# Kernel optimization log

Measured on AMD Instinct MI355X. Metric: run time of the kernel, lower is better.

Reference implementation:

```python
import jax, jax.numpy as jnp
import numpy as np

B, T, C, HS = 8, 2048, 1024, 64
SCALE = C ** (-0.5)  # NOTE: source scales by C, not head_size
NEG_INF = float('-inf')
NEG_BIG = -1e9


def setup_inputs() -> dict:
    key = jax.random.key(0)
    kV, kK, kQ, kWq, kWk, kWv, kL = jax.random.split(key, 7)
    V = jax.random.normal(kV, (B, T, C), dtype=jnp.float32)
    K = jax.random.normal(kK, (B, T, C), dtype=jnp.float32)
    Q = jax.random.normal(kQ, (B, T, C), dtype=jnp.float32)
    w_scale = 1.0 / np.sqrt(C)
    Wq = jax.random.normal(kWq, (C, HS), dtype=jnp.float32) * w_scale
    Wk = jax.random.normal(kWk, (C, HS), dtype=jnp.float32) * w_scale
    Wv = jax.random.normal(kWv, (C, HS), dtype=jnp.float32) * w_scale
    # padding only at the tail; valid lengths in [T//2, T] so no NaN softmax rows
    lengths = jax.random.randint(kL, (B,), T // 2, T + 1)
    pad_mask = (jnp.arange(T)[None, None, :] >= lengths[:, None, None])  # [B,1,T] bool
    return {"V": V, "K": K, "Q": Q, "Wq": Wq, "Wk": Wk, "Wv": Wv, "pad_mask": pad_mask}


def reference(V, K, Q, Wq, Wk, Wv, pad_mask):
    q = Q @ Wq  # [B,T,HS]
    k = K @ Wk
    v = V @ Wv
    A = jnp.einsum('btd,bsd->bts', q, k) * SCALE  # [B,T,T]
    t = A.shape[1]
    causal = jnp.triu(jnp.ones((t, A.shape[2]), dtype=bool), k=1)  # tril==0
    A = jnp.where(causal[None], NEG_INF, A)
    A = jnp.where(pad_mask, NEG_INF, A)  # mask padded key columns
    A = jnp.where(jnp.swapaxes(pad_mask, -2, -1)[:, :t, :], NEG_BIG, A)  # padded query rows
    A = jax.nn.softmax(A, axis=-1)
    return A @ v  # [B,T,HS]
```

## Files before the change

kernel.cpp:

```cpp
#include <hip/hip_runtime.h>
#include <hip/hip_bf16.h>

typedef short bf16x8 __attribute__((ext_vector_type(8)));
typedef float f32x4 __attribute__((ext_vector_type(4)));
typedef unsigned int u32;
typedef u32 u32x4 __attribute__((ext_vector_type(4)));

#define T_SEQ 2048
#define NB 8
#define NEGB (-1e30f)

__device__ inline unsigned short f2bf(float f) {
  unsigned u = __builtin_bit_cast(unsigned, f);
  u += 0x7FFFu + ((u >> 16) & 1u);
  return (unsigned short)(u >> 16);
}
__device__ inline float bf2f(unsigned short h) {
  unsigned u = ((unsigned)h) << 16;
  return __builtin_bit_cast(float, u);
}
__device__ inline u32 cvt2(float a, float b) {
  __hip_bfloat162 h = __float22bfloat162_rn(make_float2(a, b));
  u32 r;
  __builtin_memcpy(&r, &h, 4);
  return r;
}
__device__ inline bf16x8 pack8(float4 a, float4 b) {
  u32x4 p;
  p[0] = cvt2(a.x, a.y);
  p[1] = cvt2(a.z, a.w);
  p[2] = cvt2(b.x, b.y);
  p[3] = cvt2(b.z, b.w);
  return __builtin_bit_cast(bf16x8, p);
}
__device__ inline f32x4 mfma16(bf16x8 a, bf16x8 b, f32x4 c) {
  return __builtin_amdgcn_mfma_f32_16x16x32_bf16(a, b, c, 0, 0, 0);
}
__device__ __forceinline__ void gl_lds16(const void* g, void* l) {
  __builtin_amdgcn_global_load_lds(
      (const __attribute__((address_space(1))) void*)g,
      (__attribute__((address_space(3))) void*)l, 16, 0, 0);
}

__global__ void prep_k(const float* Wq, const float* Wk, const float* Wv,
                       unsigned short* wt, const unsigned char* m,
                       int* lengths, float* vmsum) {
  int tid = threadIdx.x;
  if (blockIdx.x < 768) {
    int e = blockIdx.x * 256 + tid;
    int mi = e >> 16;
    int rem = e & 65535;
    int kk = rem & 1023, n = rem >> 10;
    const float* W = (mi == 0) ? Wq : (mi == 1) ? Wk : Wv;
    wt[e] = f2bf(W[kk * 64 + n]);
    return;
  }
  int b = blockIdx.x - 768;
  if (tid < 64) vmsum[b * 64 + tid] = 0.f;
  int lo = 0, lb = 0;
  for (int i = tid; i < NB * T_SEQ; i += 256) {
    int v = (m[i] != 0);
    lo += v;
    if (i & 3) lb += v;
  }
  for (int off = 32; off >= 1; off >>= 1) {
    lo += __shfl_xor(lo, off);
    lb += __shfl_xor(lb, off);
  }
  __shared__ int s0[4], s1[4], ws2[4];
  if ((tid & 63) == 0) { s0[tid >> 6] = lo; s1[tid >> 6] = lb; }
  __syncthreads();
  int ones = s0[0] + s0[1] + s0[2] + s0[3];
  int bad = s1[0] + s1[1] + s1[2] + s1[3];
  int flag = (ones > 0 && bad == 0);
  int cnt = 0;
  if (flag) {
    const int* mi2 = (const int*)m;
    for (int t = tid; t < T_SEQ; t += 256) cnt += (mi2[b * T_SEQ + t] == 0);
  } else {
    for (int t = tid; t < T_SEQ; t += 256) cnt += (m[b * T_SEQ + t] == 0);
  }
  for (int off = 32; off >= 1; off >>= 1) cnt += __shfl_xor(cnt, off);
  __syncthreads();
  if ((tid & 63) == 0) ws2[tid >> 6] = cnt;
  __syncthreads();
  if (tid == 0) lengths[b] = ws2[0] + ws2[1] + ws2[2] + ws2[3];
}

__global__ __launch_bounds__(512, 4) void proj_k(
    const float* Q, const float* K, const float* V, const unsigned short* wt,
    unsigned short* qo, unsigned short* ko, unsigned short* vTb, float* vmsum) {
  __shared__ float xs[2][4096];
  __shared__ unsigned short wss[2][4096];
  int mi = blockIdx.y;
  const float* X = (mi == 0) ? Q : (mi == 1) ? K : V;
  const unsigned short* wtm = wt + mi * 65536;
  int tid = threadIdx.x;
  int w = tid >> 6, lane = tid & 63, l15 = lane & 15, g = lane >> 4;
  int wr = w >> 1, wc = w & 1;
  int r0b = blockIdx.x * 64;

  int segA = w * 2;
  int rowA0 = segA * 4 + (lane >> 4);
  int rowA1 = rowA0 + 4;
  int colA0 = ((lane & 15) ^ (rowA0 & 15)) * 4;
  int colA1 = ((lane & 15) ^ (rowA1 & 15)) * 4;
  const float* srcA0 = X + (size_t)(r0b + rowA0) * 1024 + colA0;
  const float* srcA1 = X + (size_t)(r0b + rowA1) * 1024 + colA1;
  int nW = w * 8 + (lane >> 3);
  int skW = ((lane & 7) ^ (nW & 7)) * 8;
  const unsigned short* srcW = wtm + (size_t)nW * 1024 + skW;

  f32x4 acc[2];
  acc[0] = 0; acc[1] = 0;

#define STAGE(buf, kc2)                                          \
  do {                                                           \
    gl_lds16(srcA0 + (kc2) * 64, &xs[buf][segA * 256]);          \
    gl_lds16(srcA1 + (kc2) * 64, &xs[buf][segA * 256 + 256]);    \
    gl_lds16(srcW + (kc2) * 64, &wss[buf][w * 512]);             \
  } while (0)

  STAGE(0, 0);

  int arow = wr * 16 + l15;
  for (int kc = 0; kc < 16; ++kc) {
    int cur = kc & 1;
    if (kc < 15) {
      STAGE(cur ^ 1, kc + 1);
      asm volatile("s_waitcnt vmcnt(3)" ::: "memory");
    } else {
      asm volatile("s_waitcnt vmcnt(0)" ::: "memory");
    }
    __builtin_amdgcn_s_barrier();
#pragma unroll
    for (int ks = 0; ks < 2; ++ks) {
      int lb0 = ks * 8 + g * 2;
      float4 fa = *(const float4*)&xs[cur][arow * 64 + ((lb0 ^ l15) * 4)];
      float4 fb = *(const float4*)&xs[cur][arow * 64 + (((lb0 + 1) ^ l15) * 4)];
      bf16x8 a = pack8(fa, fb);
#pragma unroll
      for (int nt = 0; nt < 2; ++nt) {
        int nrow = wc * 32 + nt * 16 + l15;
        bf16x8 bb = *(const bf16x8*)
            &wss[cur][nrow * 64 + (((ks * 4 + g) ^ (l15 & 7)) * 8)];
        acc[nt] = mfma16(a, bb, acc[nt]);
      }
    }
    if (kc < 15) {
      asm volatile("s_waitcnt lgkmcnt(0)" ::: "memory");
      __builtin_amdgcn_s_barrier();
    }
  }
#undef STAGE

#pragma unroll
  for (int nt = 0; nt < 2; ++nt)
#pragma unroll
    for (int vv = 0; vv < 4; ++vv) {
      int rr = r0b + wr * 16 + g * 4 + vv;
      int c = wc * 32 + nt * 16 + l15;
      float val = acc[nt][vv];
      if (mi == 0) {
        qo[(size_t)rr * 64 + c] = f2bf(val * 0.03125f);
      } else if (mi == 1) {
        ko[(size_t)rr * 64 + c] = f2bf(val);
      } else {
        int bb = rr >> 11, ts = rr & 2047;
        vTb[(((size_t)bb * 64 + (ts >> 5)) * 64 + c) * 32 + (ts & 31)] =
            f2bf(val);
      }
    }

  if (mi == 2) {
    float ps0 = acc[0][0] + acc[0][1] + acc[0][2] + acc[0][3];
    float ps1 = acc[1][0] + acc[1][1] + acc[1][2] + acc[1][3];
    __syncthreads();
    float* rb = (float*)xs;
    rb[(wc * 32 + l15) * 16 + (wr * 4 + g)] = ps0;
    rb[(wc * 32 + 16 + l15) * 16 + (wr * 4 + g)] = ps1;
    __syncthreads();
    if (tid < 64) {
      float s = 0.f;
#pragma unroll
      for (int i = 0; i < 16; ++i) s += rb[tid * 16 + i];
      atomicAdd(&vmsum[(blockIdx.x >> 5) * 64 + tid], s);
    }
  }
}

__global__ __launch_bounds__(512, 4) void attn_k(
    const unsigned short* q, const unsigned short* k, const unsigned short* vTb,
    const float* vmsum, const int* lengths, float* Out) {
  __shared__ unsigned short pL[8][16][40];
  __shared__ unsigned short oP[4][2][16][64];
  __shared__ float mP[4][2][16], lP[4][2][16];

  int id = blockIdx.x;
  int raw = id & 63, b = id >> 6;
  int xx = (raw + 8 * b) & 63;
  int tile = (xx < 32) ? xx : 95 - xx;
  int t0 = tile * 32;

  int tid = threadIdx.x;
  int w = tid >> 6, lane = tid & 63;
  int j = w >> 1, r = w & 1;
  int l15 = lane & 15, g = lane >> 4;
  int t_base = t0 + r * 16;

  const bf16x8* qrow =
      (const bf16x8*)(q + ((size_t)b * T_SEQ + t_base + l15) * 64);
  bf16x8 aq0 = qrow[g];
  bf16x8 aq1 = qrow[4 + g];

  f32x4 o[4];
  float m[4], l[4];
#pragma unroll
  for (int i = 0; i < 4; ++i) { o[i] = 0; m[i] = NEGB; l[i] = 0.f; }

  const bf16x8* kch = (const bf16x8*)k + (size_t)b * T_SEQ * 8;
  const unsigned short* vch = vTb + (size_t)b * 131072;

  int NT = tile + 1;
  int qn = NT >> 2, rem = NT & 3;
  int start = j * qn + (j < rem ? j : rem);
  int end = start + qn + (j < rem ? 1 : 0);
  int capw = ((t_base + 15) >> 5) + 1;
  if (end > capw) end = capw;

  bf16x8 kb00, kb01, kb10, kb11, bv0, bv1, bv2, bv3;
  if (start < end) {
    int s0 = start * 32;
    kb00 = kch[(size_t)(s0 + l15) * 8 + g];
    kb01 = kch[(size_t)(s0 + l15) * 8 + 4 + g];
    kb10 = kch[(size_t)(s0 + 16 + l15) * 8 + g];
    kb11 = kch[(size_t)(s0 + 16 + l15) * 8 + 4 + g];
    bv0 = *(const bf16x8*)&vch[((size_t)(start * 64 + l15)) * 32 + g * 8];
    bv1 = *(const bf16x8*)&vch[((size_t)(start * 64 + 16 + l15)) * 32 + g * 8];
    bv2 = *(const bf16x8*)&vch[((size_t)(start * 64 + 32 + l15)) * 32 + g * 8];
    bv3 = *(const bf16x8*)&vch[((size_t)(start * 64 + 48 + l15)) * 32 + g * 8];
  }

  for (int tt = start; tt < end; ++tt) {
    int s0 = tt * 32;
    f32x4 sa0, sa1;
    sa0 = 0; sa1 = 0;
    sa0 = mfma16(aq0, kb00, sa0);
    sa0 = mfma16(aq1, kb01, sa0);
    sa1 = mfma16(aq0, kb10, sa1);
    sa1 = mfma16(aq1, kb11, sa1);

    bf16x8 nk00, nk01, nk10, nk11, nv0, nv1, nv2, nv3;
    bool more = (tt + 1 < end);
    if (more) {
      int s1 = (tt + 1) * 32;
      nk00 = kch[(size_t)(s1 + l15) * 8 + g];
      nk01 = kch[(size_t)(s1 + l15) * 8 + 4 + g];
      nk10 = kch[(size_t)(s1 + 16 + l15) * 8 + g];
      nk11 = kch[(size_t)(s1 + 16 + l15) * 8 + 4 + g];
      int t1 = (tt + 1) * 64;
      nv0 = *(const bf16x8*)&vch[((size_t)(t1 + l15)) * 32 + g * 8];
      nv1 = *(const bf16x8*)&vch[((size_t)(t1 + 16 + l15)) * 32 + g * 8];
      nv2 = *(const bf16x8*)&vch[((size_t)(t1 + 32 + l15)) * 32 + g * 8];
      nv3 = *(const bf16x8*)&vch[((size_t)(t1 + 48 + l15)) * 32 + g * 8];
    }

#pragma unroll
    for (int vv = 0; vv < 4; ++vv) {
      int t = t_base + g * 4 + vv;
      float v0 = (s0 + l15 <= t) ? sa0[vv] : NEGB;
      float v1 = (s0 + 16 + l15 <= t) ? sa1[vv] : NEGB;
      float rm = fmaxf(v0, v1);
#pragma unroll
      for (int off = 8; off >= 1; off >>= 1)
        rm = fmaxf(rm, __shfl_xor(rm, off));
      float mn = fmaxf(m[vv], rm);
      float corr = __expf(m[vv] - mn);
      float p0 = (v0 == NEGB) ? 0.f : __expf(v0 - mn);
      float p1 = (v1 == NEGB) ? 0.f : __expf(v1 - mn);
      float rs = p0 + p1;
#pragma unroll
      for (int off = 8; off >= 1; off >>= 1) rs += __shfl_xor(rs, off);
      l[vv] = l[vv] * corr + rs;
      m[vv] = mn;
#pragma unroll
      for (int nt = 0; nt < 4; ++nt) o[nt][vv] *= corr;
      pL[w][g * 4 + vv][l15] = f2bf(p0);
      pL[w][g * 4 + vv][16 + l15] = f2bf(p1);
    }
    bf16x8 ap = *(const bf16x8*)&pL[w][l15][g * 8];
    o[0] = mfma16(ap, bv0, o[0]);
    o[1] = mfma16(ap, bv1, o[1]);
    o[2] = mfma16(ap, bv2, o[2]);
    o[3] = mfma16(ap, bv3, o[3]);
    if (more) {
      kb00 = nk00; kb01 = nk01; kb10 = nk10; kb11 = nk11;
      bv0 = nv0; bv1 = nv1; bv2 = nv2; bv3 = nv3;
    }
  }

  __syncthreads();
#pragma unroll
  for (int nt = 0; nt < 4; ++nt)
#pragma unroll
    for (int vv = 0; vv < 4; ++vv)
      oP[j][r][g * 4 + vv][nt * 16 + l15] = f2bf(o[nt][vv]);
  if (l15 == 0) {
#pragma unroll
    for (int vv = 0; vv < 4; ++vv) {
      mP[j][r][g * 4 + vv] = m[vv];
      lP[j][r][g * 4 + vv] = l[vv];
    }
  }
  __syncthreads();

  if (w < 2) {
    int len = lengths[b];
#pragma unroll 4
    for (int row = 0; row < 16; ++row) {
      float m0 = mP[0][w][row], m1 = mP[1][w][row];
      float m2 = mP[2][w][row], m3 = mP[3][w][row];
      float ms = fmaxf(fmaxf(m0, m1), fmaxf(m2, m3));
      float e0 = __expf(m0 - ms), e1 = __expf(m1 - ms);
      float e2 = __expf(m2 - ms), e3 = __expf(m3 - ms);
      float ls = lP[0][w][row] * e0 + lP[1][w][row] * e1 +
                 lP[2][w][row] * e2 + lP[3][w][row] * e3;
      float ov = bf2f(oP[0][w][row][lane]) * e0 +
                 bf2f(oP[1][w][row][lane]) * e1 +
                 bf2f(oP[2][w][row][lane]) * e2 +
                 bf2f(oP[3][w][row][lane]) * e3;
      float val = ov / ls;
      int t = t0 + w * 16 + row;
      if (t >= len) val = vmsum[b * 64 + lane] * (1.0f / T_SEQ);
      Out[((size_t)b * T_SEQ + t) * 64 + lane] = val;
    }
  }
}

extern "C" void kernel_launch(void* const* d_in, const int* in_sizes, int n_in,
                              void* d_out, int out_size, void* d_ws,
                              size_t ws_size, hipStream_t stream) {
  const float* V = (const float*)d_in[0];
  const float* K = (const float*)d_in[1];
  const float* Q = (const float*)d_in[2];
  const float* Wq = (const float*)d_in[3];
  const float* Wk = (const float*)d_in[4];
  const float* Wv = (const float*)d_in[5];
  const unsigned char* mask = (const unsigned char*)d_in[6];
  float* O = (float*)d_out;
  char* ws = (char*)d_ws;

  unsigned short* wt = (unsigned short*)(ws);
  unsigned short* qb = (unsigned short*)(ws + 393216);
  unsigned short* kb = (unsigned short*)(ws + 393216 + 2097152);
  unsigned short* vTb = (unsigned short*)(ws + 393216 + 2 * 2097152);
  float* vmsum = (float*)(ws + 393216 + 3 * 2097152);
  int* lengths = (int*)(ws + 393216 + 3 * 2097152 + 2048);

  prep_k<<<776, 256, 0, stream>>>(Wq, Wk, Wv, wt, mask, lengths, vmsum);
  proj_k<<<dim3(256, 3), 512, 0, stream>>>(Q, K, V, wt, qb, kb, vTb, vmsum);
  attn_k<<<512, 512, 0, stream>>>(qb, kb, vTb, vmsum, lengths, O);
}
```

Before: 82.54 us.

## Pre-swizzle weights into MFMA fragment order and spread split-K merge across all waves

The prep kernel now writes the bf16 transposed weights in MFMA B-fragment order, so the projection kernel loads each fragment straight from global memory (cache-resident) and no longer stages weights through LDS, which removes one LDS buffer and one async copy per stage. The split-K combine at the end of attention now spreads its 32 output rows over all waves at 4 rows each, instead of having two waves handle 16 rows each. The cost is global-memory B loads issued inside the inner MFMA loop, which may expose latency.

```diff
diff --git a/kernel.cpp b/kernel.cpp
--- a/kernel.cpp
+++ b/kernel.cpp
@@ -48,9 +48,13 @@
   int tid = threadIdx.x;
   if (blockIdx.x < 768) {
     int e = blockIdx.x * 256 + tid;
+    int i = e & 7;
+    int lane = (e >> 3) & 63;
+    int nt = (e >> 9) & 3;
+    int ks = (e >> 11) & 31;
     int mi = e >> 16;
-    int rem = e & 65535;
-    int kk = rem & 1023, n = rem >> 10;
+    int kk = ks * 32 + (lane >> 4) * 8 + i;
+    int n = nt * 16 + (lane & 15);
     const float* W = (mi == 0) ? Wq : (mi == 1) ? Wk : Wv;
     wt[e] = f2bf(W[kk * 64 + n]);
     return;
@@ -91,7 +95,6 @@
     const float* Q, const float* K, const float* V, const unsigned short* wt,
     unsigned short* qo, unsigned short* ko, unsigned short* vTb, float* vmsum) {
   __shared__ float xs[2][4096];
-  __shared__ unsigned short wss[2][4096];
   int mi = blockIdx.y;
   const float* X = (mi == 0) ? Q : (mi == 1) ? K : V;
   const unsigned short* wtm = wt + mi * 65536;
@@ -107,9 +110,6 @@
   int colA1 = ((lane & 15) ^ (rowA1 & 15)) * 4;
   const float* srcA0 = X + (size_t)(r0b + rowA0) * 1024 + colA0;
   const float* srcA1 = X + (size_t)(r0b + rowA1) * 1024 + colA1;
-  int nW = w * 8 + (lane >> 3);
-  int skW = ((lane & 7) ^ (nW & 7)) * 8;
-  const unsigned short* srcW = wtm + (size_t)nW * 1024 + skW;
 
   f32x4 acc[2];
   acc[0] = 0; acc[1] = 0;
@@ -118,17 +118,17 @@
   do {                                                           \
     gl_lds16(srcA0 + (kc2) * 64, &xs[buf][segA * 256]);          \
     gl_lds16(srcA1 + (kc2) * 64, &xs[buf][segA * 256 + 256]);    \
-    gl_lds16(srcW + (kc2) * 64, &wss[buf][w * 512]);             \
   } while (0)
 
   STAGE(0, 0);
 
   int arow = wr * 16 + l15;
+  const unsigned short* wfb = wtm + wc * 1024 + lane * 8;
   for (int kc = 0; kc < 16; ++kc) {
     int cur = kc & 1;
     if (kc < 15) {
       STAGE(cur ^ 1, kc + 1);
-      asm volatile("s_waitcnt vmcnt(3)" ::: "memory");
+      asm volatile("s_waitcnt vmcnt(2)" ::: "memory");
     } else {
       asm volatile("s_waitcnt vmcnt(0)" ::: "memory");
     }
@@ -139,13 +139,10 @@
       float4 fa = *(const float4*)&xs[cur][arow * 64 + ((lb0 ^ l15) * 4)];
       float4 fb = *(const float4*)&xs[cur][arow * 64 + (((lb0 + 1) ^ l15) * 4)];
       bf16x8 a = pack8(fa, fb);
-#pragma unroll
-      for (int nt = 0; nt < 2; ++nt) {
-        int nrow = wc * 32 + nt * 16 + l15;
-        bf16x8 bb = *(const bf16x8*)
-            &wss[cur][nrow * 64 + (((ks * 4 + g) ^ (l15 & 7)) * 8)];
-        acc[nt] = mfma16(a, bb, acc[nt]);
-      }
+      const bf16x8* wb =
+          (const bf16x8*)(wfb + (size_t)(kc * 2 + ks) * 2048);
+      acc[0] = mfma16(a, wb[0], acc[0]);
+      acc[1] = mfma16(a, wb[64], acc[1]);
     }
     if (kc < 15) {
       asm volatile("s_waitcnt lgkmcnt(0)" ::: "memory");
@@ -314,23 +311,25 @@
   }
   __syncthreads();
 
-  if (w < 2) {
+  {
     int len = lengths[b];
-#pragma unroll 4
-    for (int row = 0; row < 16; ++row) {
-      float m0 = mP[0][w][row], m1 = mP[1][w][row];
-      float m2 = mP[2][w][row], m3 = mP[3][w][row];
+#pragma unroll
+    for (int rr2 = 0; rr2 < 4; ++rr2) {
+      int gr = w * 4 + rr2;
+      int rq = gr >> 4, row = gr & 15;
+      float m0 = mP[0][rq][row], m1 = mP[1][rq][row];
+      float m2 = mP[2][rq][row], m3 = mP[3][rq][row];
       float ms = fmaxf(fmaxf(m0, m1), fmaxf(m2, m3));
       float e0 = __expf(m0 - ms), e1 = __expf(m1 - ms);
       float e2 = __expf(m2 - ms), e3 = __expf(m3 - ms);
-      float ls = lP[0][w][row] * e0 + lP[1][w][row] * e1 +
-                 lP[2][w][row] * e2 + lP[3][w][row] * e3;
-      float ov = bf2f(oP[0][w][row][lane]) * e0 +
-                 bf2f(oP[1][w][row][lane]) * e1 +
-                 bf2f(oP[2][w][row][lane]) * e2 +
-                 bf2f(oP[3][w][row][lane]) * e3;
+      float ls = lP[0][rq][row] * e0 + lP[1][rq][row] * e1 +
+                 lP[2][rq][row] * e2 + lP[3][rq][row] * e3;
+      float ov = bf2f(oP[0][rq][row][lane]) * e0 +
+                 bf2f(oP[1][rq][row][lane]) * e1 +
+                 bf2f(oP[2][rq][row][lane]) * e2 +
+                 bf2f(oP[3][rq][row][lane]) * e3;
       float val = ov / ls;
-      int t = t0 + w * 16 + row;
+      int t = t0 + gr;
       if (t >= len) val = vmsum[b * 64 + lane] * (1.0f / T_SEQ);
       Out[((size_t)b * T_SEQ + t) * 64 + lane] = val;
     }
```

Result: no change. 82.12 us (-0.5%).
